# Kernel optimization log

Hardware: AMD Instinct MI355X
Metric: run time of the kernel (lower is better)

## Reference

```python
import jax, jax.numpy as jnp
import numpy as np

SPATIAL = 128   # N: wall spatial resolution
CROP = 256      # M: temporal bins (power of 2)
BIN_LEN = 0.01
WALL_SIZE = 2.0


def _grids():
    # Reproduces parpareparam(): normalized freq-domain coordinate grids, [2M,2N,2N].
    M, N = CROP, SPATIAL
    width = WALL_SIZE / 2.0
    trange = CROP * BIN_LEN  # crop * c * (bin_len / c)
    zdim = (np.arange(2 * M, dtype=np.float32) - M) / M
    xdim = (np.arange(2 * N, dtype=np.float32) - N) / N
    gz = np.ascontiguousarray(np.broadcast_to(zdim[:, None, None], (2 * M, 2 * N, 2 * N)))
    gy = np.ascontiguousarray(np.broadcast_to(xdim[None, :, None], (2 * M, 2 * N, 2 * N)))
    gx = np.ascontiguousarray(np.broadcast_to(xdim[None, None, :], (2 * M, 2 * N, 2 * N)))
    fkrange = (N * trange / (M * width * 4.0)) ** 2
    gznew = np.sqrt(fkrange * (gx ** 2 + gy ** 2) + gz ** 2).astype(np.float32)
    return jnp.asarray(gx), jnp.asarray(gy), jnp.asarray(gz), jnp.asarray(gznew)


def _grid_sample_3d(vol, x, y, z):
    """Trilinear grid sample, padding_mode='zeros', align_corners=False.
    vol: [B, D, H, W] (complex ok); x/y/z: [Dg,Hg,Wg] in [-1,1] (x->W, y->H, z->D)."""
    B, D, H, W = vol.shape
    ix = ((x + 1.0) * W - 1.0) * 0.5
    iy = ((y + 1.0) * H - 1.0) * 0.5
    iz = ((z + 1.0) * D - 1.0) * 0.5
    ix0 = jnp.floor(ix); iy0 = jnp.floor(iy); iz0 = jnp.floor(iz)
    fx = ix - ix0; fy = iy - iy0; fz = iz - iz0
    ix0 = ix0.astype(jnp.int32); iy0 = iy0.astype(jnp.int32); iz0 = iz0.astype(jnp.int32)
    out = jnp.zeros((B,) + x.shape, vol.dtype)
    for dz in (0, 1):
        for dy in (0, 1):
            for dx in (0, 1):
                xi = ix0 + dx; yi = iy0 + dy; zi = iz0 + dz
                valid = (xi >= 0) & (xi < W) & (yi >= 0) & (yi < H) & (zi >= 0) & (zi < D)
                w = ((fx if dx else 1.0 - fx) * (fy if dy else 1.0 - fy) * (fz if dz else 1.0 - fz))
                w = jnp.where(valid, w, 0.0)
                xi = jnp.clip(xi, 0, W - 1); yi = jnp.clip(yi, 0, H - 1); zi = jnp.clip(zi, 0, D - 1)
                out = out + vol[:, zi, yi, xi] * w  # gather 8 trilinear corners
    return out


def _fk_forward(feat_padded):
    # feat_padded: [B, Dn, CROP, N, N] float32
    B, Dn, T, H, W = feat_padded.shape
    M, N = CROP, SPATIAL
    gx, gy, gz, gznew = _grids()
    gridz = jnp.arange(M, dtype=jnp.float32) / (M - 1)  # gridz_1xMx1x1
    data = feat_padded.reshape(B * Dn, M, N, N) * (gridz ** 2)[None, :, None, None]
    data = jax.nn.relu(data)
    # sqrt with grad-safe double-where (torch sqrt backward at 0 is nan; math limit here is 0)
    data = jnp.where(data > 0, jnp.sqrt(jnp.where(data > 0, data, 1.0)), 0.0)
    pad = jnp.zeros((B * Dn, 2 * M, 2 * N, 2 * N), jnp.float32).at[:, :M, :N, :N].set(data)
    fre = jnp.fft.fftn(pad, axes=(1, 2, 3))            # torch.rfft(x,3,onesided=False)
    fre = jnp.roll(fre, (M, N, N), axis=(1, 2, 3))      # fftshift rolls
    t = _grid_sample_3d(fre, gx, gy, gznew)             # Stolt frequency resampling
    t = t.at[:, :M + 1].set(0.0)                        # z0pos = M+1 (first zdim>0)
    t = t * (jnp.abs(gz) / (gznew + 1e-8))[None]        # |f_z| Jacobian scaling
    t = jnp.roll(t, (M, N, N), axis=(1, 2, 3))          # ifftshift (even dims)
    vol = jnp.fft.ifftn(t, axes=(1, 2, 3))[:, :M, :N, :N]
    out = vol.real ** 2 + vol.imag ** 2                 # squared magnitude
    return out.reshape(B, Dn, M, N, N)


def setup_inputs() -> dict:
    key = jax.random.key(0)
    feat = jax.random.uniform(key, (1, 1, CROP, SPATIAL, SPATIAL), dtype=jnp.float32)
    return {"feture_bxdxtxhxw": feat, "tbes": 0, "tens": CROP}


def reference(feture_bxdxtxhxw, tbes, tens):
    tbe, ten = int(tbes), int(tens)
    featpad = jnp.pad(feture_bxdxtxhxw, ((0, 0), (0, 0), (tbe, CROP - ten), (0, 0), (0, 0)))
    return _fk_forward(featpad)
```

## Files before the change

### kernel.cpp

```cpp
#include <hip/hip_runtime.h>


typedef float2 cpx;

__device__ float2 g_tw[512];

__device__ __forceinline__ cpx cadd(cpx a, cpx b){ return make_float2(a.x+b.x, a.y+b.y); }
__device__ __forceinline__ cpx csub(cpx a, cpx b){ return make_float2(a.x-b.x, a.y-b.y); }
__device__ __forceinline__ cpx cmul(cpx a, cpx b){ return make_float2(a.x*b.x - a.y*b.y, a.x*b.y + a.y*b.x); }

__global__ void k_tw(){
    int j = threadIdx.x;
    double a = -2.0*3.14159265358979323846*(double)j/512.0;
    g_tw[j] = make_float2((float)cos(a), (float)sin(a));
}

template<bool INV>
__device__ __forceinline__ cpx twmul(cpx a, int k){
    cpx w = g_tw[k & 511];
    if (INV) w.y = -w.y;
    return cmul(a, w);
}

template<bool INV>
__device__ __forceinline__ void dft4(cpx* x){
    cpx e0 = cadd(x[0], x[2]), e1 = csub(x[0], x[2]);
    cpx o0 = cadd(x[1], x[3]), o1 = csub(x[1], x[3]);
    x[0] = cadd(e0, o0);
    x[2] = csub(e0, o0);
    if (!INV){ x[1] = make_float2(e1.x + o1.y, e1.y - o1.x);
               x[3] = make_float2(e1.x - o1.y, e1.y + o1.x); }
    else     { x[1] = make_float2(e1.x - o1.y, e1.y + o1.x);
               x[3] = make_float2(e1.x + o1.y, e1.y - o1.x); }
}

template<bool INV>
__device__ __forceinline__ void dft8(cpx* x){
    const float s = 0.70710678118654752440f;
    cpx e0 = cadd(x[0], x[4]), e2 = csub(x[0], x[4]);
    cpx e1 = cadd(x[2], x[6]), e3 = csub(x[2], x[6]);
    cpx E0 = cadd(e0, e1), E2 = csub(e0, e1);
    cpx E1, E3;
    if (!INV){ E1 = make_float2(e2.x + e3.y, e2.y - e3.x);
               E3 = make_float2(e2.x - e3.y, e2.y + e3.x); }
    else     { E1 = make_float2(e2.x - e3.y, e2.y + e3.x);
               E3 = make_float2(e2.x + e3.y, e2.y - e3.x); }
    cpx o0 = cadd(x[1], x[5]), o2 = csub(x[1], x[5]);
    cpx o1 = cadd(x[3], x[7]), o3 = csub(x[3], x[7]);
    cpx O0 = cadd(o0, o1), O2 = csub(o0, o1);
    cpx O1, O3;
    if (!INV){ O1 = make_float2(o2.x + o3.y, o2.y - o3.x);
               O3 = make_float2(o2.x - o3.y, o2.y + o3.x); }
    else     { O1 = make_float2(o2.x - o3.y, o2.y + o3.x);
               O3 = make_float2(o2.x + o3.y, o2.y - o3.x); }
    cpx W1, W2, W3;
    if (!INV){
        W1 = make_float2(s*(O1.x + O1.y), s*(O1.y - O1.x));
        W2 = make_float2(O2.y, -O2.x);
        W3 = make_float2(s*(O3.y - O3.x), -s*(O3.x + O3.y));
    } else {
        W1 = make_float2(s*(O1.x - O1.y), s*(O1.x + O1.y));
        W2 = make_float2(-O2.y, O2.x);
        W3 = make_float2(-s*(O3.x + O3.y), s*(O3.x - O3.y));
    }
    x[0] = cadd(E0, O0); x[4] = csub(E0, O0);
    x[1] = cadd(E1, W1); x[5] = csub(E1, W1);
    x[2] = cadd(E2, W2); x[6] = csub(E2, W2);
    x[3] = cadd(E3, W3); x[7] = csub(E3, W3);
}

template<bool INV>
__device__ __forceinline__ void fft_rows2(cpx* s, const cpx* ltw, int tid){
    const int L2LEN = 8, LEN = 256;
    #pragma unroll
    for (int st = 0; st < L2LEN; ++st){
        int lh = L2LEN - 1 - st;
        int half = 1 << lh;
        int tws = 512 >> (L2LEN - st);
        int l  = tid >> (L2LEN - 1);
        int bf = tid & ((LEN/2) - 1);
        int j  = bf & (half - 1);
        int i0 = ((bf >> lh) << (lh + 1)) | j;
        cpx u = s[l*LEN + i0], v = s[l*LEN + i0 + half];
        cpx w = ltw[j*tws];
        if (INV) w.y = -w.y;
        s[l*LEN + i0]        = cadd(u, v);
        s[l*LEN + i0 + half] = cmul(csub(u, v), w);
        __syncthreads();
    }
    for (int i = tid; i < 2*LEN; i += 256){
        int l = i >> L2LEN, k = i & (LEN - 1);
        int r = __brev((unsigned)k) >> (32 - L2LEN);
        if (r > k){ cpx a = s[l*LEN + k]; s[l*LEN + k] = s[l*LEN + r]; s[l*LEN + r] = a; }
    }
    __syncthreads();
}

__global__ __launch_bounds__(256) void k_fft_x_fill(const float* __restrict__ feat, cpx* __restrict__ V){
    __shared__ cpx s[2*256];
    __shared__ cpx ltw[256];
    int tid = threadIdx.x;
    ltw[tid] = g_tw[tid];
    int line0 = blockIdx.x << 1;
    {
        int l = tid >> 7, e = tid & 127;
        int line = line0 + l;
        int z = line >> 7;
        float g = (float)z*(1.0f/255.0f);
        float v = feat[(line << 7) + e]*g*g;
        v = v > 0.0f ? sqrtf(v) : 0.0f;
        s[l*256 + e]       = make_float2(v, 0.0f);
        s[l*256 + e + 128] = make_float2(0.0f, 0.0f);
    }
    __syncthreads();
    fft_rows2<false>(s, ltw, tid);
    {
        int l = tid >> 7, f = tid & 127;
        int line = line0 + l;
        int base = ((line >> 7) << 16) + ((line & 127) << 8);
        const float4* srow = (const float4*)(s + l*256);
        float4 A = srow[f ^ 64];
        float4 B = make_float4(0.0f, 0.0f, 0.0f, 0.0f);
        if (f) B = srow[(f - 1) ^ 64];
        float4 o;
        o.x = 0.5f*(B.z + A.x); o.y = 0.5f*(B.w + A.y);
        o.z = 0.5f*(A.x + A.z); o.w = 0.5f*(A.y + A.w);
        ((float4*)(V + base))[f] = o;
    }
}

__global__ __launch_bounds__(256) void k_fft_x_inv_mag(const cpx* __restrict__ W,
                                                       float* __restrict__ out){
    __shared__ cpx s[2*256];
    __shared__ cpx ltw[256];
    int tid = threadIdx.x;
    ltw[tid] = g_tw[tid];
    int line0 = blockIdx.x << 1;
    {
        int l = tid >> 7, f4c = tid & 127;
        int line = line0 + l;
        int base = ((line >> 7) << 16) + ((line & 127) << 8);
        ((float4*)(s + l*256))[f4c] = ((const float4*)(W + base))[f4c];
    }
    __syncthreads();
    fft_rows2<true>(s, ltw, tid);
    {
        int l = tid >> 7, e = tid & 127;
        int line = line0 + l;
        int z = line >> 7, y = line & 127;
        cpx v = s[l*256 + e];
        const float SC2 = (1.0f/33554432.0f)*(1.0f/33554432.0f);
        out[(z*128 + y)*128 + e] = (v.x*v.x + v.y*v.y)*SC2;
    }
}

template<bool INV, bool HALF_IN, bool HALF_OUT>
__global__ __launch_bounds__(1024) void k_fft_y(cpx* __restrict__ V){
    __shared__ cpx s[256*16];
    int tid = threadIdx.x;
    int z  = blockIdx.x >> 4;
    int x0 = (blockIdx.x & 15) << 4;
    int base = (z << 16) + x0;
    const int YIN = HALF_IN ? 128 : 256;
    for (int i = tid; i < YIN*8; i += 1024){
        int f4c = i & 7, e = i >> 3;
        ((float4*)(s + e*16))[f4c] = ((const float4*)(V + base + (e << 8)))[f4c];
    }
    if (HALF_IN){
        for (int i = tid; i < 128*16; i += 1024){
            int c = i & 15, e = (i >> 4) + 128;
            s[e*16 + c] = make_float2(0.0f, 0.0f);
        }
    }
    __syncthreads();
    int c = tid & 15, idx = tid >> 4;
    cpx x[4];
    {
        int j = idx;
        #pragma unroll
        for (int t = 0; t < 4; ++t) x[t] = s[(j + (t << 6))*16 + c];
        dft4<INV>(x);
        #pragma unroll
        for (int r = 1; r < 4; ++r) x[r] = twmul<INV>(x[r], 2*j*r);
        #pragma unroll
        for (int r = 0; r < 4; ++r) s[(j + (r << 6))*16 + c] = x[r];
    }
    __syncthreads();
    {
        int j = idx & 15, g = (idx >> 4) << 6;
        #pragma unroll
        for (int t = 0; t < 4; ++t) x[t] = s[(g + j + (t << 4))*16 + c];
        dft4<INV>(x);
        #pragma unroll
        for (int r = 1; r < 4; ++r) x[r] = twmul<INV>(x[r], 8*j*r);
        #pragma unroll
        for (int r = 0; r < 4; ++r) s[(g + j + (r << 4))*16 + c] = x[r];
    }
    __syncthreads();
    {
        int j = idx & 3, g = (idx >> 2) << 4;
        #pragma unroll
        for (int t = 0; t < 4; ++t) x[t] = s[(g + j + (t << 2))*16 + c];
        dft4<INV>(x);
        #pragma unroll
        for (int r = 1; r < 4; ++r) x[r] = twmul<INV>(x[r], 32*j*r);
        #pragma unroll
        for (int r = 0; r < 4; ++r) s[(g + j + (r << 2))*16 + c] = x[r];
    }
    __syncthreads();
    {
        int g = idx << 2;
        #pragma unroll
        for (int t = 0; t < 4; ++t) x[t] = s[(g + t)*16 + c];
        dft4<INV>(x);
        #pragma unroll
        for (int r = 0; r < 4; ++r) s[(g + r)*16 + c] = x[r];
    }
    __syncthreads();
    const int YOUT = HALF_OUT ? 128 : 256;
    for (int i = tid; i < YOUT*8; i += 1024){
        int f4c = i & 7, e = i >> 3;
        if (!INV){
            int p0 = (((e & 3) << 6) | (((e >> 2) & 3) << 4) | (((e >> 4) & 3) << 2) | (e >> 6)) ^ 2;
            float4 S0 = ((const float4*)(s + p0*16))[f4c];
            float4 S1 = make_float4(0.0f, 0.0f, 0.0f, 0.0f);
            if (e){
                int em = e - 1;
                int p1 = (((em & 3) << 6) | (((em >> 2) & 3) << 4) | (((em >> 4) & 3) << 2) | (em >> 6)) ^ 2;
                S1 = ((const float4*)(s + p1*16))[f4c];
            }
            float4 o;
            o.x = 0.5f*(S0.x + S1.x); o.y = 0.5f*(S0.y + S1.y);
            o.z = 0.5f*(S0.z + S1.z); o.w = 0.5f*(S0.w + S1.w);
            ((float4*)(V + base + (e << 8)))[f4c] = o;
        } else {
            int p = ((e & 3) << 6) | (((e >> 2) & 3) << 4) | (((e >> 4) & 3) << 2) | (e >> 6);
            ((float4*)(V + base + (e << 8)))[f4c] = ((const float4*)(s + p*16))[f4c];
        }
    }
}

__global__ __launch_bounds__(1024) void k_fft_z_fwd(cpx* __restrict__ V){
    __shared__ cpx s[512*16];
    int tid = threadIdx.x;
    int y  = blockIdx.x >> 4;
    int x0 = (blockIdx.x & 15) << 4;
    int base = (y << 8) + x0;
    for (int i = tid; i < 256*8; i += 1024){
        int f4c = i & 7, e = i >> 3;
        ((float4*)(s + e*16))[f4c] = ((const float4*)(V + base + (e << 16)))[f4c];
    }
    for (int i = tid; i < 256*16; i += 1024){
        int c = i & 15, e = (i >> 4) + 256;
        s[e*16 + c] = make_float2(0.0f, 0.0f);
    }
    __syncthreads();
    int c = tid & 15, idx = tid >> 4;
    cpx x[8];
    {
        int j = idx;
        #pragma unroll
        for (int t = 0; t < 8; ++t) x[t] = s[(j + (t << 6))*16 + c];
        dft8<false>(x);
        #pragma unroll
        for (int r = 1; r < 8; ++r) x[r] = twmul<false>(x[r], j*r);
        #pragma unroll
        for (int r = 0; r < 8; ++r) s[(j + (r << 6))*16 + c] = x[r];
    }
    __syncthreads();
    {
        int j = idx & 7, g = (idx >> 3) << 6;
        #pragma unroll
        for (int t = 0; t < 8; ++t) x[t] = s[(g + j + (t << 3))*16 + c];
        dft8<false>(x);
        #pragma unroll
        for (int r = 1; r < 8; ++r) x[r] = twmul<false>(x[r], 8*j*r);
        #pragma unroll
        for (int r = 0; r < 8; ++r) s[(g + j + (r << 3))*16 + c] = x[r];
    }
    __syncthreads();
    {
        int g = idx << 3;
        #pragma unroll
        for (int t = 0; t < 8; ++t) x[t] = s[(g + t)*16 + c];
        dft8<false>(x);
        #pragma unroll
        for (int r = 0; r < 8; ++r) s[(g + r)*16 + c] = x[r];
    }
    __syncthreads();
    for (int i = tid; i < 256*8; i += 1024){
        int f4c = i & 7, e = i >> 3;
        int p = ((e & 7) << 6) | (e & 56) | (e >> 6);
        ((float4*)(V + base + ((e + 256) << 16)))[f4c] = ((const float4*)(s + p*16))[f4c];
    }
}

__global__ __launch_bounds__(1024) void k_stolt_fftz_inv(const cpx* __restrict__ Vsrc, cpx* __restrict__ V){
    __shared__ cpx s[512*16];
    int tid = threadIdx.x;
    int y  = blockIdx.x >> 4;
    int x0 = (blockIdx.x & 15) << 4;
    int base = (y << 8) + x0;
    int c = tid & 15;
    int xd = x0 + c;
    int xs = (xd + 128) & 255;
    int ys = (y + 128) & 255;
    float gx = (float)(xs - 128)*(1.0f/128.0f);
    float gy = (float)(ys - 128)*(1.0f/128.0f);
    float rxy = 0.1024f*(gx*gx + gy*gy);
    int srcoff = (ys << 8) + xs;
    #pragma unroll 4
    for (int i = tid; i < 256*16; i += 1024){
        int zd = i >> 4;
        cpx r = make_float2(0.0f, 0.0f);
        if (zd){
            float gz = (float)zd*(1.0f/256.0f);
            float gzn = sqrtf(rxy + gz*gz);
            float iz = ((gzn + 1.0f)*512.0f - 1.0f)*0.5f;
            float fiz = floorf(iz);
            int iz0 = (int)fiz;
            float fz = iz - fiz;
            float sc = gz/(gzn + 1e-8f);
            int z0 = iz0 < 511 ? iz0 : 511;
            int z1 = (iz0 + 1) < 511 ? (iz0 + 1) : 511;
            float wz0 = (iz0     <= 511) ? (1.0f - fz)*sc : 0.0f;
            float wz1 = (iz0 + 1 <= 511) ? fz*sc : 0.0f;
            cpx a = Vsrc[((size_t)z0 << 16) + srcoff];
            cpx b = Vsrc[((size_t)z1 << 16) + srcoff];
            r.x = a.x*wz0 + b.x*wz1;
            r.y = a.y*wz0 + b.y*wz1;
        }
        s[i] = r;
    }
    for (int i = tid; i < 256*16; i += 1024){
        int cc = i & 15, e = (i >> 4) + 256;
        s[e*16 + cc] = make_float2(0.0f, 0.0f);
    }
    __syncthreads();
    int idx = tid >> 4;
    cpx x[8];
    {
        int j = idx;
        #pragma unroll
        for (int t = 0; t < 8; ++t) x[t] = s[(j + (t << 6))*16 + c];
        dft8<true>(x);
        #pragma unroll
        for (int r = 1; r < 8; ++r) x[r] = twmul<true>(x[r], j*r);
        #pragma unroll
        for (int r = 0; r < 8; ++r) s[(j + (r << 6))*16 + c] = x[r];
    }
    __syncthreads();
    {
        int j = idx & 7, g = (idx >> 3) << 6;
        #pragma unroll
        for (int t = 0; t < 8; ++t) x[t] = s[(g + j + (t << 3))*16 + c];
        dft8<true>(x);
        #pragma unroll
        for (int r = 1; r < 8; ++r) x[r] = twmul<true>(x[r], 8*j*r);
        #pragma unroll
        for (int r = 0; r < 8; ++r) s[(g + j + (r << 3))*16 + c] = x[r];
    }
    __syncthreads();
    {
        int g = idx << 3;
        #pragma unroll
        for (int t = 0; t < 8; ++t) x[t] = s[(g + t)*16 + c];
        dft8<true>(x);
        #pragma unroll
        for (int r = 0; r < 8; ++r) s[(g + r)*16 + c] = x[r];
    }
    __syncthreads();
    for (int i = tid; i < 256*8; i += 1024){
        int f4c = i & 7, e = i >> 3;
        int p = ((e & 7) << 6) | (e & 56) | (e >> 6);
        ((float4*)(V + base + (e << 16)))[f4c] = ((const float4*)(s + p*16))[f4c];
    }
}

extern "C" void kernel_launch(void* const* d_in, const int* in_sizes, int n_in,
                              void* d_out, int out_size, void* d_ws, size_t ws_size,
                              hipStream_t stream){
    const float* feat = (const float*)d_in[0];
    float* out = (float*)d_out;

    const size_t WS_NEED = (size_t)512*256*256*8;
    if (ws_size < WS_NEED){
        hipMemsetAsync(d_out, 0, (size_t)out_size*sizeof(float), stream);
        return;
    }
    cpx* V = (cpx*)d_ws;

    k_tw<<<1, 512, 0, stream>>>();
    k_fft_x_fill<<<16384, 256, 0, stream>>>(feat, V);
    k_fft_y<false, true, false><<<4096, 1024, 0, stream>>>(V);
    k_fft_z_fwd<<<4096, 1024, 0, stream>>>(V);
    k_stolt_fftz_inv<<<4096, 1024, 0, stream>>>(V, V);
    k_fft_y<true, false, true><<<4096, 1024, 0, stream>>>(V);
    k_fft_x_inv_mag<<<16384, 256, 0, stream>>>(V, out);
}
```

Baseline: 305.8 us.

## Fuse forward z-FFT, Stolt resampling and inverse z-FFT into paired-column kernel

Merges the forward z-FFT kernel and the Stolt-interpolation-plus-inverse-z-FFT kernel into one. Each block loads a column tile and its fftshift partner tile, since the Stolt gather for one reads the other. It runs the forward FFT on both in shared memory, resamples from shared memory, runs the inverse FFT and writes back. This removes the global write and re-read of the 512-deep forward spectrum and the scattered global gathers. In exchange each block uses 128 KB of shared memory and half as many blocks are launched, which lowers occupancy.

```diff
diff --git a/kernel.cpp b/kernel.cpp
--- a/kernel.cpp
+++ b/kernel.cpp
@@ -69,6 +69,57 @@
     x[3] = cadd(E3, W3); x[7] = csub(E3, W3);
 }
 
+template<bool INV, int STAGE>
+__device__ __forceinline__ void zstage(cpx* s, int c, int idx){
+    cpx x[8];
+    if (STAGE == 0){
+        int j = idx;
+        #pragma unroll
+        for (int t = 0; t < 8; ++t) x[t] = s[(j + (t << 6))*16 + c];
+        dft8<INV>(x);
+        #pragma unroll
+        for (int r = 1; r < 8; ++r) x[r] = twmul<INV>(x[r], j*r);
+        #pragma unroll
+        for (int r = 0; r < 8; ++r) s[(j + (r << 6))*16 + c] = x[r];
+    } else if (STAGE == 1){
+        int j = idx & 7, g = (idx >> 3) << 6;
+        #pragma unroll
+        for (int t = 0; t < 8; ++t) x[t] = s[(g + j + (t << 3))*16 + c];
+        dft8<INV>(x);
+        #pragma unroll
+        for (int r = 1; r < 8; ++r) x[r] = twmul<INV>(x[r], 8*j*r);
+        #pragma unroll
+        for (int r = 0; r < 8; ++r) s[(g + j + (r << 3))*16 + c] = x[r];
+    } else {
+        int g = idx << 3;
+        #pragma unroll
+        for (int t = 0; t < 8; ++t) x[t] = s[(g + t)*16 + c];
+        dft8<INV>(x);
+        #pragma unroll
+        for (int r = 0; r < 8; ++r) s[(g + r)*16 + c] = x[r];
+    }
+}
+
+__device__ __forceinline__ cpx zgather(const cpx* __restrict__ buf, int zd, float rxy, int c){
+    if (!zd) return make_float2(0.0f, 0.0f);
+    float gz = (float)zd*(1.0f/256.0f);
+    float gzn = sqrtf(rxy + gz*gz);
+    float iz = ((gzn + 1.0f)*512.0f - 1.0f)*0.5f;
+    float fiz = floorf(iz);
+    int iz0 = (int)fiz;
+    float fz = iz - fiz;
+    float sc = gz/(gzn + 1e-8f);
+    int b0 = (iz0 < 511 ? iz0 : 511) - 256;
+    int b1 = ((iz0 + 1) < 511 ? (iz0 + 1) : 511) - 256;
+    float w0 = (iz0     <= 511) ? (1.0f - fz)*sc : 0.0f;
+    float w1 = (iz0 + 1 <= 511) ? fz*sc : 0.0f;
+    int p0 = ((b0 & 7) << 6) | (b0 & 56) | (b0 >> 6);
+    int p1 = ((b1 & 7) << 6) | (b1 & 56) | (b1 >> 6);
+    cpx a = buf[p0*16 + c];
+    cpx b = buf[p1*16 + c];
+    return make_float2(a.x*w0 + b.x*w1, a.y*w0 + b.y*w1);
+}
+
 template<bool INV>
 __device__ __forceinline__ void fft_rows2(cpx* s, const cpx* ltw, int tid){
     const int L2LEN = 8, LEN = 256;
@@ -240,140 +291,65 @@
     }
 }
 
-__global__ __launch_bounds__(1024) void k_fft_z_fwd(cpx* __restrict__ V){
-    __shared__ cpx s[512*16];
+__global__ __launch_bounds__(1024) void k_fftz_pair(cpx* __restrict__ V){
+    __shared__ cpx bufA[512*16];
+    __shared__ cpx bufB[512*16];
     int tid = threadIdx.x;
-    int y  = blockIdx.x >> 4;
-    int x0 = (blockIdx.x & 15) << 4;
-    int base = (y << 8) + x0;
+    int yA  = blockIdx.x >> 4;
+    int x0A = (blockIdx.x & 15) << 4;
+    int yB  = yA + 128;
+    int x0B = (x0A + 128) & 255;
+    int baseA = (yA << 8) + x0A;
+    int baseB = (yB << 8) + x0B;
     for (int i = tid; i < 256*8; i += 1024){
         int f4c = i & 7, e = i >> 3;
-        ((float4*)(s + e*16))[f4c] = ((const float4*)(V + base + (e << 16)))[f4c];
+        ((float4*)(bufA + e*16))[f4c] = ((const float4*)(V + baseA + (e << 16)))[f4c];
+        ((float4*)(bufB + e*16))[f4c] = ((const float4*)(V + baseB + (e << 16)))[f4c];
     }
     for (int i = tid; i < 256*16; i += 1024){
-        int c = i & 15, e = (i >> 4) + 256;
-        s[e*16 + c] = make_float2(0.0f, 0.0f);
+        int cc = i & 15, e = (i >> 4) + 256;
+        bufA[e*16 + cc] = make_float2(0.0f, 0.0f);
+        bufB[e*16 + cc] = make_float2(0.0f, 0.0f);
     }
     __syncthreads();
     int c = tid & 15, idx = tid >> 4;
-    cpx x[8];
-    {
-        int j = idx;
-        #pragma unroll
-        for (int t = 0; t < 8; ++t) x[t] = s[(j + (t << 6))*16 + c];
-        dft8<false>(x);
-        #pragma unroll
-        for (int r = 1; r < 8; ++r) x[r] = twmul<false>(x[r], j*r);
-        #pragma unroll
-        for (int r = 0; r < 8; ++r) s[(j + (r << 6))*16 + c] = x[r];
-    }
-    __syncthreads();
-    {
-        int j = idx & 7, g = (idx >> 3) << 6;
-        #pragma unroll
-        for (int t = 0; t < 8; ++t) x[t] = s[(g + j + (t << 3))*16 + c];
-        dft8<false>(x);
-        #pragma unroll
-        for (int r = 1; r < 8; ++r) x[r] = twmul<false>(x[r], 8*j*r);
-        #pragma unroll
-        for (int r = 0; r < 8; ++r) s[(g + j + (r << 3))*16 + c] = x[r];
-    }
-    __syncthreads();
-    {
-        int g = idx << 3;
-        #pragma unroll
-        for (int t = 0; t < 8; ++t) x[t] = s[(g + t)*16 + c];
-        dft8<false>(x);
-        #pragma unroll
-        for (int r = 0; r < 8; ++r) s[(g + r)*16 + c] = x[r];
-    }
-    __syncthreads();
+    zstage<false,0>(bufA, c, idx); zstage<false,0>(bufB, c, idx); __syncthreads();
+    zstage<false,1>(bufA, c, idx); zstage<false,1>(bufB, c, idx); __syncthreads();
+    zstage<false,2>(bufA, c, idx); zstage<false,2>(bufB, c, idx); __syncthreads();
+    float gxA = (float)(x0B + c - 128)*(1.0f/128.0f);
+    float gyA = (float)(yB - 128)*(1.0f/128.0f);
+    float rxyA = 0.1024f*(gxA*gxA + gyA*gyA);
+    float gxB = (float)(x0A + c - 128)*(1.0f/128.0f);
+    float gyB = (float)(yA - 128)*(1.0f/128.0f);
+    float rxyB = 0.1024f*(gxB*gxB + gyB*gyB);
+    cpx rA[4], rB[4];
+    #pragma unroll
+    for (int k = 0; k < 4; ++k){
+        int zd = idx + (k << 6);
+        rA[k] = zgather(bufB, zd, rxyA, c);
+        rB[k] = zgather(bufA, zd, rxyB, c);
+    }
+    __syncthreads();
+    #pragma unroll
+    for (int k = 0; k < 4; ++k){
+        int zd = idx + (k << 6);
+        bufA[zd*16 + c] = rA[k];
+        bufB[zd*16 + c] = rB[k];
+    }
+    for (int i = tid; i < 256*16; i += 1024){
+        int cc = i & 15, e = (i >> 4) + 256;
+        bufA[e*16 + cc] = make_float2(0.0f, 0.0f);
+        bufB[e*16 + cc] = make_float2(0.0f, 0.0f);
+    }
+    __syncthreads();
+    zstage<true,0>(bufA, c, idx); zstage<true,0>(bufB, c, idx); __syncthreads();
+    zstage<true,1>(bufA, c, idx); zstage<true,1>(bufB, c, idx); __syncthreads();
+    zstage<true,2>(bufA, c, idx); zstage<true,2>(bufB, c, idx); __syncthreads();
     for (int i = tid; i < 256*8; i += 1024){
         int f4c = i & 7, e = i >> 3;
         int p = ((e & 7) << 6) | (e & 56) | (e >> 6);
-        ((float4*)(V + base + ((e + 256) << 16)))[f4c] = ((const float4*)(s + p*16))[f4c];
-    }
-}
-
-__global__ __launch_bounds__(1024) void k_stolt_fftz_inv(const cpx* __restrict__ Vsrc, cpx* __restrict__ V){
-    __shared__ cpx s[512*16];
-    int tid = threadIdx.x;
-    int y  = blockIdx.x >> 4;
-    int x0 = (blockIdx.x & 15) << 4;
-    int base = (y << 8) + x0;
-    int c = tid & 15;
-    int xd = x0 + c;
-    int xs = (xd + 128) & 255;
-    int ys = (y + 128) & 255;
-    float gx = (float)(xs - 128)*(1.0f/128.0f);
-    float gy = (float)(ys - 128)*(1.0f/128.0f);
-    float rxy = 0.1024f*(gx*gx + gy*gy);
-    int srcoff = (ys << 8) + xs;
-    #pragma unroll 4
-    for (int i = tid; i < 256*16; i += 1024){
-        int zd = i >> 4;
-        cpx r = make_float2(0.0f, 0.0f);
-        if (zd){
-            float gz = (float)zd*(1.0f/256.0f);
-            float gzn = sqrtf(rxy + gz*gz);
-            float iz = ((gzn + 1.0f)*512.0f - 1.0f)*0.5f;
-            float fiz = floorf(iz);
-            int iz0 = (int)fiz;
-            float fz = iz - fiz;
-            float sc = gz/(gzn + 1e-8f);
-            int z0 = iz0 < 511 ? iz0 : 511;
-            int z1 = (iz0 + 1) < 511 ? (iz0 + 1) : 511;
-            float wz0 = (iz0     <= 511) ? (1.0f - fz)*sc : 0.0f;
-            float wz1 = (iz0 + 1 <= 511) ? fz*sc : 0.0f;
-            cpx a = Vsrc[((size_t)z0 << 16) + srcoff];
-            cpx b = Vsrc[((size_t)z1 << 16) + srcoff];
-            r.x = a.x*wz0 + b.x*wz1;
-            r.y = a.y*wz0 + b.y*wz1;
-        }
-        s[i] = r;
-    }
-    for (int i = tid; i < 256*16; i += 1024){
-        int cc = i & 15, e = (i >> 4) + 256;
-        s[e*16 + cc] = make_float2(0.0f, 0.0f);
-    }
-    __syncthreads();
-    int idx = tid >> 4;
-    cpx x[8];
-    {
-        int j = idx;
-        #pragma unroll
-        for (int t = 0; t < 8; ++t) x[t] = s[(j + (t << 6))*16 + c];
-        dft8<true>(x);
-        #pragma unroll
-        for (int r = 1; r < 8; ++r) x[r] = twmul<true>(x[r], j*r);
-        #pragma unroll
-        for (int r = 0; r < 8; ++r) s[(j + (r << 6))*16 + c] = x[r];
-    }
-    __syncthreads();
-    {
-        int j = idx & 7, g = (idx >> 3) << 6;
-        #pragma unroll
-        for (int t = 0; t < 8; ++t) x[t] = s[(g + j + (t << 3))*16 + c];
-        dft8<true>(x);
-        #pragma unroll
-        for (int r = 1; r < 8; ++r) x[r] = twmul<true>(x[r], 8*j*r);
-        #pragma unroll
-        for (int r = 0; r < 8; ++r) s[(g + j + (r << 3))*16 + c] = x[r];
-    }
-    __syncthreads();
-    {
-        int g = idx << 3;
-        #pragma unroll
-        for (int t = 0; t < 8; ++t) x[t] = s[(g + t)*16 + c];
-        dft8<true>(x);
-        #pragma unroll
-        for (int r = 0; r < 8; ++r) s[(g + r)*16 + c] = x[r];
-    }
-    __syncthreads();
-    for (int i = tid; i < 256*8; i += 1024){
-        int f4c = i & 7, e = i >> 3;
-        int p = ((e & 7) << 6) | (e & 56) | (e >> 6);
-        ((float4*)(V + base + (e << 16)))[f4c] = ((const float4*)(s + p*16))[f4c];
+        ((float4*)(V + baseA + (e << 16)))[f4c] = ((const float4*)(bufA + p*16))[f4c];
+        ((float4*)(V + baseB + (e << 16)))[f4c] = ((const float4*)(bufB + p*16))[f4c];
     }
 }
 
@@ -393,8 +369,7 @@
     k_tw<<<1, 512, 0, stream>>>();
     k_fft_x_fill<<<16384, 256, 0, stream>>>(feat, V);
     k_fft_y<false, true, false><<<4096, 1024, 0, stream>>>(V);
-    k_fft_z_fwd<<<4096, 1024, 0, stream>>>(V);
-    k_stolt_fftz_inv<<<4096, 1024, 0, stream>>>(V, V);
+    k_fftz_pair<<<2048, 1024, 0, stream>>>(V);
     k_fft_y<true, false, true><<<4096, 1024, 0, stream>>>(V);
     k_fft_x_inv_mag<<<16384, 256, 0, stream>>>(V, out);
 }
```

Result: slower. 313.8 us (+2.6%).

## Replace radix-2 x-axis FFT with radix-4 and process four lines per block

Applied to the files above, without the earlier changes.

Replaces the eight-stage radix-2 shared-memory FFT used for the x-axis forward and inverse passes with a four-stage radix-4 FFT, using global twiddles and digit-reversed indexing instead of a bit-reversal swap pass. Each block now handles four 256-point lines with 64 threads per line, halving the grid size and using vectorized float2 loads and stores. This cuts barriers and shared-memory passes per line, at the cost of more register work per thread and scattered digit-reversed shared reads. The Stolt gather is also factored into a helper with no behavioral change.

```diff
diff --git a/kernel.cpp b/kernel.cpp
--- a/kernel.cpp
+++ b/kernel.cpp
@@ -8,6 +8,10 @@
 __device__ __forceinline__ cpx cadd(cpx a, cpx b){ return make_float2(a.x+b.x, a.y+b.y); }
 __device__ __forceinline__ cpx csub(cpx a, cpx b){ return make_float2(a.x-b.x, a.y-b.y); }
 __device__ __forceinline__ cpx cmul(cpx a, cpx b){ return make_float2(a.x*b.x - a.y*b.y, a.x*b.y + a.y*b.x); }
+
+__device__ __forceinline__ int rev4_8(int k){
+    return ((k & 3) << 6) | ((k & 12) << 2) | ((k >> 2) & 12) | (k >> 6);
+}
 
 __global__ void k_tw(){
     int j = threadIdx.x;
@@ -70,87 +74,113 @@
 }
 
 template<bool INV>
-__device__ __forceinline__ void fft_rows2(cpx* s, const cpx* ltw, int tid){
-    const int L2LEN = 8, LEN = 256;
-    #pragma unroll
-    for (int st = 0; st < L2LEN; ++st){
-        int lh = L2LEN - 1 - st;
-        int half = 1 << lh;
-        int tws = 512 >> (L2LEN - st);
-        int l  = tid >> (L2LEN - 1);
-        int bf = tid & ((LEN/2) - 1);
-        int j  = bf & (half - 1);
-        int i0 = ((bf >> lh) << (lh + 1)) | j;
-        cpx u = s[l*LEN + i0], v = s[l*LEN + i0 + half];
-        cpx w = ltw[j*tws];
-        if (INV) w.y = -w.y;
-        s[l*LEN + i0]        = cadd(u, v);
-        s[l*LEN + i0 + half] = cmul(csub(u, v), w);
-        __syncthreads();
-    }
-    for (int i = tid; i < 2*LEN; i += 256){
-        int l = i >> L2LEN, k = i & (LEN - 1);
-        int r = __brev((unsigned)k) >> (32 - L2LEN);
-        if (r > k){ cpx a = s[l*LEN + k]; s[l*LEN + k] = s[l*LEN + r]; s[l*LEN + r] = a; }
+__device__ __forceinline__ void fft256_r4(cpx* sl, int b){
+    cpx x[4];
+    {
+        int j = b;
+        #pragma unroll
+        for (int t = 0; t < 4; ++t) x[t] = sl[j + (t << 6)];
+        dft4<INV>(x);
+        #pragma unroll
+        for (int r = 1; r < 4; ++r) x[r] = twmul<INV>(x[r], 2*j*r);
+        #pragma unroll
+        for (int r = 0; r < 4; ++r) sl[j + (r << 6)] = x[r];
+    }
+    __syncthreads();
+    {
+        int j = b & 15, g = (b >> 4) << 6;
+        #pragma unroll
+        for (int t = 0; t < 4; ++t) x[t] = sl[g + j + (t << 4)];
+        dft4<INV>(x);
+        #pragma unroll
+        for (int r = 1; r < 4; ++r) x[r] = twmul<INV>(x[r], 8*j*r);
+        #pragma unroll
+        for (int r = 0; r < 4; ++r) sl[g + j + (r << 4)] = x[r];
+    }
+    __syncthreads();
+    {
+        int j = b & 3, g = (b >> 2) << 4;
+        #pragma unroll
+        for (int t = 0; t < 4; ++t) x[t] = sl[g + j + (t << 2)];
+        dft4<INV>(x);
+        #pragma unroll
+        for (int r = 1; r < 4; ++r) x[r] = twmul<INV>(x[r], 32*j*r);
+        #pragma unroll
+        for (int r = 0; r < 4; ++r) sl[g + j + (r << 2)] = x[r];
+    }
+    __syncthreads();
+    {
+        int g = b << 2;
+        #pragma unroll
+        for (int t = 0; t < 4; ++t) x[t] = sl[g + t];
+        dft4<INV>(x);
+        #pragma unroll
+        for (int r = 0; r < 4; ++r) sl[g + r] = x[r];
     }
     __syncthreads();
 }
 
 __global__ __launch_bounds__(256) void k_fft_x_fill(const float* __restrict__ feat, cpx* __restrict__ V){
-    __shared__ cpx s[2*256];
-    __shared__ cpx ltw[256];
+    __shared__ cpx s[4*256];
     int tid = threadIdx.x;
-    ltw[tid] = g_tw[tid];
-    int line0 = blockIdx.x << 1;
-    {
-        int l = tid >> 7, e = tid & 127;
+    int line0 = blockIdx.x << 2;
+    {
+        int l = tid >> 6, e2 = tid & 63;
         int line = line0 + l;
         int z = line >> 7;
         float g = (float)z*(1.0f/255.0f);
-        float v = feat[(line << 7) + e]*g*g;
-        v = v > 0.0f ? sqrtf(v) : 0.0f;
-        s[l*256 + e]       = make_float2(v, 0.0f);
-        s[l*256 + e + 128] = make_float2(0.0f, 0.0f);
-    }
-    __syncthreads();
-    fft_rows2<false>(s, ltw, tid);
-    {
-        int l = tid >> 7, f = tid & 127;
+        float2 v = ((const float2*)(feat + ((size_t)line << 7)))[e2];
+        float a = v.x*g*g, bb = v.y*g*g;
+        a  = a  > 0.0f ? sqrtf(a)  : 0.0f;
+        bb = bb > 0.0f ? sqrtf(bb) : 0.0f;
+        cpx* sl = s + l*256;
+        sl[2*e2]       = make_float2(a, 0.0f);
+        sl[2*e2 + 1]   = make_float2(bb, 0.0f);
+        sl[128 + 2*e2]     = make_float2(0.0f, 0.0f);
+        sl[128 + 2*e2 + 1] = make_float2(0.0f, 0.0f);
+    }
+    __syncthreads();
+    fft256_r4<false>(s + (tid >> 6)*256, tid & 63);
+    for (int i = tid; i < 4*128; i += 256){
+        int l = i >> 7, f4 = i & 127;
         int line = line0 + l;
         int base = ((line >> 7) << 16) + ((line & 127) << 8);
-        const float4* srow = (const float4*)(s + l*256);
-        float4 A = srow[f ^ 64];
-        float4 B = make_float4(0.0f, 0.0f, 0.0f, 0.0f);
-        if (f) B = srow[(f - 1) ^ 64];
+        const cpx* sl = s + l*256;
+        int e0 = 2*f4;
+        cpx Fm = e0 ? sl[rev4_8(e0 - 1) ^ 2] : make_float2(0.0f, 0.0f);
+        cpx F0 = sl[rev4_8(e0) ^ 2];
+        cpx F1 = sl[rev4_8(e0 + 1) ^ 2];
         float4 o;
-        o.x = 0.5f*(B.z + A.x); o.y = 0.5f*(B.w + A.y);
-        o.z = 0.5f*(A.x + A.z); o.w = 0.5f*(A.y + A.w);
-        ((float4*)(V + base))[f] = o;
+        o.x = 0.5f*(Fm.x + F0.x); o.y = 0.5f*(Fm.y + F0.y);
+        o.z = 0.5f*(F0.x + F1.x); o.w = 0.5f*(F0.y + F1.y);
+        ((float4*)(V + base))[f4] = o;
     }
 }
 
 __global__ __launch_bounds__(256) void k_fft_x_inv_mag(const cpx* __restrict__ W,
                                                        float* __restrict__ out){
-    __shared__ cpx s[2*256];
-    __shared__ cpx ltw[256];
+    __shared__ cpx s[4*256];
     int tid = threadIdx.x;
-    ltw[tid] = g_tw[tid];
-    int line0 = blockIdx.x << 1;
-    {
-        int l = tid >> 7, f4c = tid & 127;
+    int line0 = blockIdx.x << 2;
+    for (int i = tid; i < 4*128; i += 256){
+        int l = i >> 7, f4 = i & 127;
         int line = line0 + l;
         int base = ((line >> 7) << 16) + ((line & 127) << 8);
-        ((float4*)(s + l*256))[f4c] = ((const float4*)(W + base))[f4c];
-    }
-    __syncthreads();
-    fft_rows2<true>(s, ltw, tid);
-    {
-        int l = tid >> 7, e = tid & 127;
+        ((float4*)(s + l*256))[f4] = ((const float4*)(W + base))[f4];
+    }
+    __syncthreads();
+    fft256_r4<true>(s + (tid >> 6)*256, tid & 63);
+    {
+        int l = tid >> 6, e2 = tid & 63;
         int line = line0 + l;
         int z = line >> 7, y = line & 127;
-        cpx v = s[l*256 + e];
+        const cpx* sl = s + l*256;
+        cpx v0 = sl[rev4_8(2*e2)];
+        cpx v1 = sl[rev4_8(2*e2 + 1)];
         const float SC2 = (1.0f/33554432.0f)*(1.0f/33554432.0f);
-        out[(z*128 + y)*128 + e] = (v.x*v.x + v.y*v.y)*SC2;
+        float2 o = make_float2((v0.x*v0.x + v0.y*v0.y)*SC2,
+                               (v1.x*v1.x + v1.y*v1.y)*SC2);
+        ((float2*)(out + (((size_t)(z*128 + y)) << 7)))[e2] = o;
     }
 }
 
@@ -221,12 +251,11 @@
     for (int i = tid; i < YOUT*8; i += 1024){
         int f4c = i & 7, e = i >> 3;
         if (!INV){
-            int p0 = (((e & 3) << 6) | (((e >> 2) & 3) << 4) | (((e >> 4) & 3) << 2) | (e >> 6)) ^ 2;
+            int p0 = rev4_8(e) ^ 2;
             float4 S0 = ((const float4*)(s + p0*16))[f4c];
             float4 S1 = make_float4(0.0f, 0.0f, 0.0f, 0.0f);
             if (e){
-                int em = e - 1;
-                int p1 = (((em & 3) << 6) | (((em >> 2) & 3) << 4) | (((em >> 4) & 3) << 2) | (em >> 6)) ^ 2;
+                int p1 = rev4_8(e - 1) ^ 2;
                 S1 = ((const float4*)(s + p1*16))[f4c];
             }
             float4 o;
@@ -234,7 +263,7 @@
             o.z = 0.5f*(S0.z + S1.z); o.w = 0.5f*(S0.w + S1.w);
             ((float4*)(V + base + (e << 8)))[f4c] = o;
         } else {
-            int p = ((e & 3) << 6) | (((e >> 2) & 3) << 4) | (((e >> 4) & 3) << 2) | (e >> 6);
+            int p = rev4_8(e);
             ((float4*)(V + base + (e << 8)))[f4c] = ((const float4*)(s + p*16))[f4c];
         }
     }
@@ -293,6 +322,24 @@
         int p = ((e & 7) << 6) | (e & 56) | (e >> 6);
         ((float4*)(V + base + ((e + 256) << 16)))[f4c] = ((const float4*)(s + p*16))[f4c];
     }
+}
+
+__device__ __forceinline__ cpx zgather_g(const cpx* __restrict__ Vsrc, int zd, float rxy, int srcoff){
+    if (!zd) return make_float2(0.0f, 0.0f);
+    float gz = (float)zd*(1.0f/256.0f);
+    float gzn = sqrtf(rxy + gz*gz);
+    float iz = ((gzn + 1.0f)*512.0f - 1.0f)*0.5f;
+    float fiz = floorf(iz);
+    int iz0 = (int)fiz;
+    float fz = iz - fiz;
+    float sc = gz/(gzn + 1e-8f);
+    int z0 = iz0 < 511 ? iz0 : 511;
+    int z1 = (iz0 + 1) < 511 ? (iz0 + 1) : 511;
+    float w0 = (iz0     <= 511) ? (1.0f - fz)*sc : 0.0f;
+    float w1 = (iz0 + 1 <= 511) ? fz*sc : 0.0f;
+    cpx a = Vsrc[((size_t)z0 << 16) + srcoff];
+    cpx b = Vsrc[((size_t)z1 << 16) + srcoff];
+    return make_float2(a.x*w0 + b.x*w1, a.y*w0 + b.y*w1);
 }
 
 __global__ __launch_bounds__(1024) void k_stolt_fftz_inv(const cpx* __restrict__ Vsrc, cpx* __restrict__ V){
@@ -312,25 +359,7 @@
     #pragma unroll 4
     for (int i = tid; i < 256*16; i += 1024){
         int zd = i >> 4;
-        cpx r = make_float2(0.0f, 0.0f);
-        if (zd){
-            float gz = (float)zd*(1.0f/256.0f);
-            float gzn = sqrtf(rxy + gz*gz);
-            float iz = ((gzn + 1.0f)*512.0f - 1.0f)*0.5f;
-            float fiz = floorf(iz);
-            int iz0 = (int)fiz;
-            float fz = iz - fiz;
-            float sc = gz/(gzn + 1e-8f);
-            int z0 = iz0 < 511 ? iz0 : 511;
-            int z1 = (iz0 + 1) < 511 ? (iz0 + 1) : 511;
-            float wz0 = (iz0     <= 511) ? (1.0f - fz)*sc : 0.0f;
-            float wz1 = (iz0 + 1 <= 511) ? fz*sc : 0.0f;
-            cpx a = Vsrc[((size_t)z0 << 16) + srcoff];
-            cpx b = Vsrc[((size_t)z1 << 16) + srcoff];
-            r.x = a.x*wz0 + b.x*wz1;
-            r.y = a.y*wz0 + b.y*wz1;
-        }
-        s[i] = r;
+        s[i] = zgather_g(Vsrc, zd, rxy, srcoff);
     }
     for (int i = tid; i < 256*16; i += 1024){
         int cc = i & 15, e = (i >> 4) + 256;
@@ -391,10 +420,10 @@
     cpx* V = (cpx*)d_ws;
 
     k_tw<<<1, 512, 0, stream>>>();
-    k_fft_x_fill<<<16384, 256, 0, stream>>>(feat, V);
+    k_fft_x_fill<<<8192, 256, 0, stream>>>(feat, V);
     k_fft_y<false, true, false><<<4096, 1024, 0, stream>>>(V);
     k_fft_z_fwd<<<4096, 1024, 0, stream>>>(V);
     k_stolt_fftz_inv<<<4096, 1024, 0, stream>>>(V, V);
     k_fft_y<true, false, true><<<4096, 1024, 0, stream>>>(V);
-    k_fft_x_inv_mag<<<16384, 256, 0, stream>>>(V, out);
-}
+    k_fft_x_inv_mag<<<8192, 256, 0, stream>>>(V, out);
+}
```

New measurement: 281.2 us. -8.1%, faster.
